# Performance work log

Measured on AMD Instinct MI355X. Metric: run time of the kernel, lower is better.

Reference implementation:

```python
import jax, jax.numpy as jnp
import numpy as np

B, T, E = 4, 2048, 1024
NH = 16
HS = E // NH  # 64


def setup_inputs() -> dict:
    key = jax.random.key(0)
    k1, k2, k3 = jax.random.split(key, 3)
    x = jax.random.normal(k1, (B, T, E), dtype=jnp.float32)
    # nn.Linear weights, stored as [in, out] so forward is x @ W
    W_attn = jax.random.normal(k2, (E, 3 * E), dtype=jnp.float32) * (1.0 / np.sqrt(E))
    W_proj = jax.random.normal(k3, (E, E), dtype=jnp.float32) * (1.0 / np.sqrt(E))
    return {"x": x, "W_attn": W_attn, "W_proj": W_proj}


def reference(x, W_attn, W_proj):
    b, t, e = x.shape
    # qkv projection; rearrange 'b t (a nh hs) -> a b nh t hs'
    qkv = x @ W_attn                                  # [b, t, 3e]
    qkv = qkv.reshape(b, t, 3, NH, HS)
    qkv = jnp.transpose(qkv, (2, 0, 3, 1, 4))          # [3, b, nh, t, hs]
    q, k, v = qkv[0], qkv[1], qkv[2]

    scale = 1.0 / np.sqrt(HS)
    # the blocked online-softmax loop in the original computes exactly
    # dense causal softmax attention
    scores = jnp.einsum('bhqd,bhkd->bhqk', q * scale, k)  # [b, nh, t, t]
    causal = jnp.tril(jnp.ones((t, t), dtype=bool))
    scores = jnp.where(causal, scores, -jnp.inf)
    p = jax.nn.softmax(scores, axis=-1)
    o = jnp.einsum('bhqk,bhkd->bhqd', p, v)            # [b, nh, t, hs]

    y = jnp.transpose(o, (0, 2, 1, 3)).reshape(b, t, e)  # 'b nh t hs -> b t (nh hs)'
    return y @ W_proj
```

## Files before the change

kernel.cpp:

```cpp
#include <hip/hip_runtime.h>
#include <hip/hip_bf16.h>
#include <cstdint>


typedef __attribute__((ext_vector_type(8))) short short8;
typedef __attribute__((ext_vector_type(4))) float f32x4;

__device__ __forceinline__ f32x4 mfma16(short8 a, short8 b, f32x4 c) {
  return __builtin_amdgcn_mfma_f32_16x16x32_bf16(a, b, c, 0, 0, 0);
}

__device__ __forceinline__ void gload16(const void* g, void* l) {
  __builtin_amdgcn_global_load_lds(
      (const __attribute__((address_space(1))) unsigned int*)g,
      (__attribute__((address_space(3))) unsigned int*)l, 16, 0, 0);
}

__device__ __forceinline__ unsigned short f2bf(float f) {
  unsigned u = __float_as_uint(f);
  u += 0x7fff + ((u >> 16) & 1);
  return (unsigned short)(u >> 16);
}

__device__ __forceinline__ float fexp2(float x) {
  float r;
  asm("v_exp_f32 %0, %1" : "=v"(r) : "v"(x));
  return r;
}

__global__ void cvt_x_kernel(const float* __restrict__ in,
                             unsigned short* __restrict__ out, int n4) {
  int i = blockIdx.x * blockDim.x + threadIdx.x;
  if (i >= n4) return;
  float4 v = ((const float4*)in)[i];
  ushort4 o;
  o.x = f2bf(v.x); o.y = f2bf(v.y); o.z = f2bf(v.z); o.w = f2bf(v.w);
  ((ushort4*)out)[i] = o;
}

__global__ void transpose_cvt_kernel(const float* __restrict__ W,
                                     unsigned short* __restrict__ Wt,
                                     int K, int N) {
  __shared__ float tile[32][33];
  int n0 = blockIdx.x * 32, k0 = blockIdx.y * 32;
  int tx = threadIdx.x, ty = threadIdx.y;
#pragma unroll
  for (int i = 0; i < 32; i += 8)
    tile[ty + i][tx] = W[(size_t)(k0 + ty + i) * N + n0 + tx];
  __syncthreads();
#pragma unroll
  for (int i = 0; i < 32; i += 8)
    Wt[(size_t)(n0 + ty + i) * K + k0 + tx] = f2bf(tile[tx][ty + i]);
}

template <int OUTF32>
__global__ __launch_bounds__(256) void gemm_bt_kernel(
    const unsigned short* __restrict__ A, const unsigned short* __restrict__ Bt,
    void* __restrict__ C, int M, int N, int K) {
  __shared__ __align__(16) unsigned short As[128 * 64];
  __shared__ __align__(16) unsigned short Bs[128 * 64];
  const int tid = threadIdx.x;
  const int lane = tid & 63;
  const int w = tid >> 6;
  const int wr = w >> 1, wc = w & 1;
  const int l15 = lane & 15, g = lane >> 4;
  const int m0 = blockIdx.x * 128, n0 = blockIdx.y * 128;

  f32x4 acc[4][4];
#pragma unroll
  for (int m = 0; m < 4; ++m)
#pragma unroll
    for (int n = 0; n < 4; ++n) acc[m][n] = (f32x4){0.f, 0.f, 0.f, 0.f};

  for (int k0 = 0; k0 < K; k0 += 64) {
    __syncthreads();
#pragma unroll
    for (int i = 0; i < 4; ++i) {
      int c = tid + 256 * i;
      int row = c >> 3;
      int piece = (c & 7) ^ (row & 7);
      gload16(A + (size_t)(m0 + row) * K + k0 + piece * 8, (char*)As + c * 16);
      gload16(Bt + (size_t)(n0 + row) * K + k0 + piece * 8, (char*)Bs + c * 16);
    }
    asm volatile("s_waitcnt vmcnt(0)" ::: "memory");
    __syncthreads();

#pragma unroll
    for (int kk = 0; kk < 2; ++kk) {
      short8 av[4], bv[4];
#pragma unroll
      for (int m = 0; m < 4; ++m) {
        int row = wr * 64 + m * 16 + l15;
        av[m] = *(const short8*)((const char*)As + row * 128 +
                                 ((kk * 64 + g * 16) ^ ((row & 7) << 4)));
      }
#pragma unroll
      for (int n = 0; n < 4; ++n) {
        int row = wc * 64 + n * 16 + l15;
        bv[n] = *(const short8*)((const char*)Bs + row * 128 +
                                 ((kk * 64 + g * 16) ^ ((row & 7) << 4)));
      }
#pragma unroll
      for (int m = 0; m < 4; ++m)
#pragma unroll
        for (int n = 0; n < 4; ++n)
          acc[m][n] = mfma16(av[m], bv[n], acc[m][n]);
    }
  }

#pragma unroll
  for (int m = 0; m < 4; ++m)
#pragma unroll
    for (int n = 0; n < 4; ++n)
#pragma unroll
      for (int r = 0; r < 4; ++r) {
        size_t row = (size_t)(m0 + wr * 64 + m * 16 + g * 4 + r);
        size_t col = (size_t)(n0 + wc * 64 + n * 16 + l15);
        if (OUTF32)
          ((float*)C)[row * N + col] = acc[m][n][r];
        else
          ((unsigned short*)C)[row * N + col] = f2bf(acc[m][n][r]);
      }
}

#define SCL 0.18033688f

__global__ __launch_bounds__(256) void attn_kernel(
    const unsigned short* __restrict__ qkv, unsigned short* __restrict__ o) {
  const int rb = blockIdx.x;
  const int lid = (rb & 7) * 128 + (rb >> 3);
  const int qt = lid & 15;
  const int bh = lid >> 4;
  const int b = bh >> 4, h = bh & 15;
  const int tid = threadIdx.x;
  const int w = tid >> 6, lane = tid & 63;
  const int l15 = lane & 15, g = lane >> 4;
  const int q0 = qt * 128;
  const int qb0 = q0 + w * 32;
  const int qb1 = qb0 + 16;

  __shared__ __align__(16) unsigned short Ks[2][64 * 64];
  __shared__ __align__(16) unsigned short Vt[2][64 * 72];
  __shared__ __align__(16) unsigned short Pl[4][32 * 72];

  const size_t row0 = (size_t)b * 2048;

  short8 qf[2][2];
#pragma unroll
  for (int u = 0; u < 2; ++u) {
    const unsigned short* qp =
        qkv + (row0 + qb0 + u * 16 + l15) * 3072 + h * 64;
#pragma unroll
    for (int c = 0; c < 2; ++c) qf[u][c] = *(const short8*)(qp + c * 32 + g * 8);
  }

  f32x4 accO[2][4];
#pragma unroll
  for (int u = 0; u < 2; ++u)
#pragma unroll
    for (int n = 0; n < 4; ++n) accO[u][n] = (f32x4){0.f, 0.f, 0.f, 0.f};
  float lsum[2] = {0.f, 0.f};

  const int kvv = (tid & 31) * 2;
  const int dv = (tid >> 5) * 8;
  const int nt = 2 * qt + 2;

  auto stageK = [&](int buf, int kt) {
#pragma unroll
    for (int i = 0; i < 2; ++i) {
      int c = tid + 256 * i;
      int row = c >> 3;
      int piece = (c & 7) ^ (row & 7);
      gload16(qkv + (row0 + kt * 64 + row) * 3072 + 1024 + h * 64 + piece * 8,
              (char*)Ks[buf] + c * 16);
    }
  };
  auto loadV = [&](int kt, short8& r0, short8& r1) {
    const unsigned short* vs =
        qkv + (row0 + kt * 64 + kvv) * 3072 + 2048 + h * 64 + dv;
    r0 = *(const short8*)vs;
    r1 = *(const short8*)(vs + 3072);
  };
  auto packV = [&](int buf, short8 r0, short8 r1) {
#pragma unroll
    for (int j = 0; j < 8; ++j) {
      unsigned pk = (unsigned)(unsigned short)r0[j] |
                    ((unsigned)(unsigned short)r1[j] << 16);
      *(unsigned*)((char*)Vt[buf] + (dv + j) * 144 + kvv * 2) = pk;
    }
  };

  short8 vr0, vr1;
  stageK(0, 0);
  loadV(0, vr0, vr1);
  asm volatile("s_waitcnt vmcnt(0)" ::: "memory");
  packV(0, vr0, vr1);

  for (int kt = 0; kt < nt; ++kt) {
    const int cur = kt & 1;
    __syncthreads();
    const bool pre = (kt + 1 < nt);
    if (pre) {
      stageK(cur ^ 1, kt + 1);
      loadV(kt + 1, vr0, vr1);
    }

    const int ktb = kt * 64;
    const bool act0 = (ktb <= qb0 + 15);
    const bool act1 = (ktb <= qb1 + 15);

    if (act1) {
      f32x4 st[2][4];
#pragma unroll
      for (int u = 0; u < 2; ++u)
#pragma unroll
        for (int tt = 0; tt < 4; ++tt) st[u][tt] = (f32x4){0.f, 0.f, 0.f, 0.f};
      const char* ksc = (const char*)Ks[cur];
#pragma unroll
      for (int tt = 0; tt < 4; ++tt) {
        int row = tt * 16 + l15;
        const char* base = ksc + row * 128;
        int sw = (row & 7) << 4;
        short8 a0 = *(const short8*)(base + ((g * 16) ^ sw));
        short8 a1 = *(const short8*)(base + ((64 + g * 16) ^ sw));
        if (act0) {
          st[0][tt] = mfma16(a0, qf[0][0], st[0][tt]);
          st[0][tt] = mfma16(a1, qf[0][1], st[0][tt]);
        }
        st[1][tt] = mfma16(a0, qf[1][0], st[1][tt]);
        st[1][tt] = mfma16(a1, qf[1][1], st[1][tt]);
      }

#pragma unroll
      for (int u = 0; u < 2; ++u) {
        const int qbu = qb0 + u * 16;
        if (ktb > qbu + 15) continue;
        const bool msk = (ktb + 63 > qbu);
        const int qq = qbu + l15;
        float part = 0.f;
#pragma unroll
        for (int tt = 0; tt < 4; ++tt) {
          float p[4];
#pragma unroll
          for (int r = 0; r < 4; ++r) {
            float s = st[u][tt][r] * SCL;
            if (msk && (ktb + tt * 16 + 4 * g + r > qq)) s = -1e30f;
            p[r] = fexp2(s);
            part += p[r];
          }
          uint2 pk;
          pk.x = (unsigned)f2bf(p[0]) | ((unsigned)f2bf(p[1]) << 16);
          pk.y = (unsigned)f2bf(p[2]) | ((unsigned)f2bf(p[3]) << 16);
          *(uint2*)((char*)Pl[w] + (u * 16 + l15) * 144 + tt * 32 + g * 8) = pk;
        }
        lsum[u] += part;
      }

#pragma unroll
      for (int c2 = 0; c2 < 2; ++c2) {
        short8 vf[4];
#pragma unroll
        for (int n = 0; n < 4; ++n)
          vf[n] = *(const short8*)((const char*)Vt[cur] +
                                   (n * 16 + l15) * 144 + c2 * 64 + g * 16);
        if (act0) {
          short8 pf0 = *(const short8*)((const char*)Pl[w] + l15 * 144 +
                                        c2 * 64 + g * 16);
#pragma unroll
          for (int n = 0; n < 4; ++n) accO[0][n] = mfma16(pf0, vf[n], accO[0][n]);
        }
        short8 pf1 = *(const short8*)((const char*)Pl[w] + (16 + l15) * 144 +
                                      c2 * 64 + g * 16);
#pragma unroll
        for (int n = 0; n < 4; ++n) accO[1][n] = mfma16(pf1, vf[n], accO[1][n]);
      }
    }

    if (pre) {
      asm volatile("s_waitcnt vmcnt(0)" ::: "memory");
      packV(cur ^ 1, vr0, vr1);
    }
  }

#pragma unroll
  for (int u = 0; u < 2; ++u) {
    float l = lsum[u];
    l += __shfl_xor(l, 16);
    l += __shfl_xor(l, 32);
    float linv[4];
#pragma unroll
    for (int r = 0; r < 4; ++r)
      linv[r] = 1.f / __shfl(l, (lane & 48) + g * 4 + r);
#pragma unroll
    for (int n = 0; n < 4; ++n)
#pragma unroll
      for (int r = 0; r < 4; ++r) {
        size_t row = row0 + qb0 + u * 16 + g * 4 + r;
        o[row * 1024 + h * 64 + n * 16 + l15] = f2bf(accO[u][n][r] * linv[r]);
      }
  }
}

extern "C" void kernel_launch(void* const* d_in, const int* in_sizes, int n_in,
                              void* d_out, int out_size, void* d_ws,
                              size_t ws_size, hipStream_t stream) {
  const float* x = (const float*)d_in[0];
  const float* W_attn = (const float*)d_in[1];
  const float* W_proj = (const float*)d_in[2];
  float* out = (float*)d_out;

  char* ws = (char*)d_ws;
  unsigned short* xb  = (unsigned short*)(ws);
  unsigned short* Wta = (unsigned short*)(ws + (16u << 20));
  unsigned short* Wtp = (unsigned short*)(ws + (22u << 20));
  unsigned short* qkv = (unsigned short*)(ws + (24u << 20));

  cvt_x_kernel<<<8192, 256, 0, stream>>>(x, xb, 8192 * 1024 / 4);
  transpose_cvt_kernel<<<dim3(96, 32), dim3(32, 8), 0, stream>>>(W_attn, Wta,
                                                                 1024, 3072);
  transpose_cvt_kernel<<<dim3(32, 32), dim3(32, 8), 0, stream>>>(W_proj, Wtp,
                                                                 1024, 1024);
  gemm_bt_kernel<0><<<dim3(64, 24), 256, 0, stream>>>(xb, Wta, qkv, 8192, 3072,
                                                      1024);
  attn_kernel<<<1024, 256, 0, stream>>>(qkv, xb);
  gemm_bt_kernel<1><<<dim3(64, 8), 256, 0, stream>>>(xb, Wtp, out, 8192, 1024,
                                                     1024);
}
```

Baseline: 283.4 us.

## Emit V transposed from QKV GEMM and restructure attention to load K/V from global

```diff
diff --git a/kernel.cpp b/kernel.cpp
--- a/kernel.cpp
+++ b/kernel.cpp
@@ -25,6 +25,12 @@
 __device__ __forceinline__ float fexp2(float x) {
   float r;
   asm("v_exp_f32 %0, %1" : "=v"(r) : "v"(x));
+  return r;
+}
+
+__device__ __forceinline__ unsigned cvtpk(float lo, float hi) {
+  unsigned r;
+  asm("v_cvt_pk_bf16_f32 %0, %1, %2" : "=v"(r) : "v"(lo), "v"(hi));
   return r;
 }
 
@@ -40,7 +46,7 @@
 
 __global__ void transpose_cvt_kernel(const float* __restrict__ W,
                                      unsigned short* __restrict__ Wt,
-                                     int K, int N) {
+                                     int K, int N, float qs, int nscale) {
   __shared__ float tile[32][33];
   int n0 = blockIdx.x * 32, k0 = blockIdx.y * 32;
   int tx = threadIdx.x, ty = threadIdx.y;
@@ -49,14 +55,19 @@
     tile[ty + i][tx] = W[(size_t)(k0 + ty + i) * N + n0 + tx];
   __syncthreads();
 #pragma unroll
-  for (int i = 0; i < 32; i += 8)
-    Wt[(size_t)(n0 + ty + i) * K + k0 + tx] = f2bf(tile[tx][ty + i]);
-}
-
-template <int OUTF32>
+  for (int i = 0; i < 32; i += 8) {
+    int n = n0 + ty + i;
+    float v = tile[tx][ty + i];
+    if (n < nscale) v *= qs;
+    Wt[(size_t)n * K + k0 + tx] = f2bf(v);
+  }
+}
+
+template <int OUTF32, int VT>
 __global__ __launch_bounds__(256) void gemm_bt_kernel(
     const unsigned short* __restrict__ A, const unsigned short* __restrict__ Bt,
-    void* __restrict__ C, int M, int N, int K) {
+    void* __restrict__ C, unsigned short* __restrict__ Cv,
+    int M, int N, int K, int ldc) {
   __shared__ __align__(16) unsigned short As[128 * 64];
   __shared__ __align__(16) unsigned short Bs[128 * 64];
   const int tid = threadIdx.x;
@@ -108,177 +119,136 @@
     }
   }
 
-#pragma unroll
-  for (int m = 0; m < 4; ++m)
-#pragma unroll
-    for (int n = 0; n < 4; ++n)
-#pragma unroll
-      for (int r = 0; r < 4; ++r) {
-        size_t row = (size_t)(m0 + wr * 64 + m * 16 + g * 4 + r);
-        size_t col = (size_t)(n0 + wc * 64 + n * 16 + l15);
-        if (OUTF32)
-          ((float*)C)[row * N + col] = acc[m][n][r];
-        else
-          ((unsigned short*)C)[row * N + col] = f2bf(acc[m][n][r]);
-      }
-}
-
-#define SCL 0.18033688f
-
-__global__ __launch_bounds__(256) void attn_kernel(
-    const unsigned short* __restrict__ qkv, unsigned short* __restrict__ o) {
+  if (!VT || n0 < 2048) {
+#pragma unroll
+    for (int m = 0; m < 4; ++m)
+#pragma unroll
+      for (int n = 0; n < 4; ++n)
+#pragma unroll
+        for (int r = 0; r < 4; ++r) {
+          size_t row = (size_t)(m0 + wr * 64 + m * 16 + g * 4 + r);
+          size_t col = (size_t)(n0 + wc * 64 + n * 16 + l15);
+          if (OUTF32)
+            ((float*)C)[row * ldc + col] = acc[m][n][r];
+          else
+            ((unsigned short*)C)[row * ldc + col] = f2bf(acc[m][n][r]);
+        }
+  } else {
+#pragma unroll
+    for (int m = 0; m < 4; ++m)
+#pragma unroll
+      for (int n = 0; n < 4; ++n)
+#pragma unroll
+        for (int r = 0; r < 4; ++r) {
+          int row = m0 + wr * 64 + m * 16 + g * 4 + r;
+          int col = n0 + wc * 64 + n * 16 + l15 - 2048;
+          int bb = row >> 11, t = row & 2047;
+          size_t dst = ((size_t)(bb * 16 + (col >> 6)) * 64 + (col & 63)) * 2048 + t;
+          Cv[dst] = f2bf(acc[m][n][r]);
+        }
+  }
+}
+
+__global__ __launch_bounds__(256, 4) void attn_kernel(
+    const unsigned short* __restrict__ qk,
+    const unsigned short* __restrict__ vt,
+    unsigned short* __restrict__ o) {
   const int rb = blockIdx.x;
-  const int lid = (rb & 7) * 128 + (rb >> 3);
-  const int qt = lid & 15;
-  const int bh = lid >> 4;
+  const int xcd = rb & 7, jj = (rb >> 3) & 31, rr = rb >> 8;
+  const int bh = xcd * 8 + (jj & 3) * 2 + (rr & 1);
+  const int pp = jj >> 2;
+  const int qt = (rr < 2) ? (15 - pp) : pp;
   const int b = bh >> 4, h = bh & 15;
   const int tid = threadIdx.x;
   const int w = tid >> 6, lane = tid & 63;
   const int l15 = lane & 15, g = lane >> 4;
-  const int q0 = qt * 128;
-  const int qb0 = q0 + w * 32;
-  const int qb1 = qb0 + 16;
-
-  __shared__ __align__(16) unsigned short Ks[2][64 * 64];
-  __shared__ __align__(16) unsigned short Vt[2][64 * 72];
+  const int qb0 = qt * 128 + w * 32;
+
   __shared__ __align__(16) unsigned short Pl[4][32 * 72];
+  char* pw = (char*)&Pl[w][0];
 
   const size_t row0 = (size_t)b * 2048;
 
   short8 qf[2][2];
 #pragma unroll
   for (int u = 0; u < 2; ++u) {
-    const unsigned short* qp =
-        qkv + (row0 + qb0 + u * 16 + l15) * 3072 + h * 64;
+    const unsigned short* qp = qk + (row0 + qb0 + u * 16 + l15) * 2048 + h * 64;
 #pragma unroll
     for (int c = 0; c < 2; ++c) qf[u][c] = *(const short8*)(qp + c * 32 + g * 8);
   }
 
-  f32x4 accO[2][4];
+  f32x4 acc[2][4];
 #pragma unroll
   for (int u = 0; u < 2; ++u)
 #pragma unroll
-    for (int n = 0; n < 4; ++n) accO[u][n] = (f32x4){0.f, 0.f, 0.f, 0.f};
+    for (int n = 0; n < 4; ++n) acc[u][n] = (f32x4){0.f, 0.f, 0.f, 0.f};
   float lsum[2] = {0.f, 0.f};
 
-  const int kvv = (tid & 31) * 2;
-  const int dv = (tid >> 5) * 8;
-  const int nt = 2 * qt + 2;
-
-  auto stageK = [&](int buf, int kt) {
-#pragma unroll
-    for (int i = 0; i < 2; ++i) {
-      int c = tid + 256 * i;
-      int row = c >> 3;
-      int piece = (c & 7) ^ (row & 7);
-      gload16(qkv + (row0 + kt * 64 + row) * 3072 + 1024 + h * 64 + piece * 8,
-              (char*)Ks[buf] + c * 16);
-    }
-  };
-  auto loadV = [&](int kt, short8& r0, short8& r1) {
-    const unsigned short* vs =
-        qkv + (row0 + kt * 64 + kvv) * 3072 + 2048 + h * 64 + dv;
-    r0 = *(const short8*)vs;
-    r1 = *(const short8*)(vs + 3072);
-  };
-  auto packV = [&](int buf, short8 r0, short8 r1) {
-#pragma unroll
-    for (int j = 0; j < 8; ++j) {
-      unsigned pk = (unsigned)(unsigned short)r0[j] |
-                    ((unsigned)(unsigned short)r1[j] << 16);
-      *(unsigned*)((char*)Vt[buf] + (dv + j) * 144 + kvv * 2) = pk;
-    }
-  };
-
-  short8 vr0, vr1;
-  stageK(0, 0);
-  loadV(0, vr0, vr1);
-  asm volatile("s_waitcnt vmcnt(0)" ::: "memory");
-  packV(0, vr0, vr1);
+  const unsigned short* kb = qk + (row0 + l15) * 2048 + 1024 + h * 64 + g * 8;
+  const unsigned short* vb = vt + ((size_t)bh * 64 + l15) * 2048 + g * 8;
+  const int nt = 2 * qt + 1 + (w >> 1);
 
   for (int kt = 0; kt < nt; ++kt) {
-    const int cur = kt & 1;
-    __syncthreads();
-    const bool pre = (kt + 1 < nt);
-    if (pre) {
-      stageK(cur ^ 1, kt + 1);
-      loadV(kt + 1, vr0, vr1);
-    }
-
     const int ktb = kt * 64;
-    const bool act0 = (ktb <= qb0 + 15);
-    const bool act1 = (ktb <= qb1 + 15);
-
-    if (act1) {
-      f32x4 st[2][4];
-#pragma unroll
-      for (int u = 0; u < 2; ++u)
-#pragma unroll
-        for (int tt = 0; tt < 4; ++tt) st[u][tt] = (f32x4){0.f, 0.f, 0.f, 0.f};
-      const char* ksc = (const char*)Ks[cur];
+    short8 kf[4][2];
+#pragma unroll
+    for (int tt = 0; tt < 4; ++tt)
+#pragma unroll
+      for (int c = 0; c < 2; ++c)
+        kf[tt][c] = *(const short8*)(kb + (size_t)(ktb + tt * 16) * 2048 + c * 32);
+
+    f32x4 st[4];
+    short8 vf[4][2];
+
+#pragma unroll
+    for (int u = 0; u < 2; ++u) {
 #pragma unroll
       for (int tt = 0; tt < 4; ++tt) {
-        int row = tt * 16 + l15;
-        const char* base = ksc + row * 128;
-        int sw = (row & 7) << 4;
-        short8 a0 = *(const short8*)(base + ((g * 16) ^ sw));
-        short8 a1 = *(const short8*)(base + ((64 + g * 16) ^ sw));
-        if (act0) {
-          st[0][tt] = mfma16(a0, qf[0][0], st[0][tt]);
-          st[0][tt] = mfma16(a1, qf[0][1], st[0][tt]);
+        st[tt] = mfma16(kf[tt][0], qf[u][0], (f32x4){0.f, 0.f, 0.f, 0.f});
+        st[tt] = mfma16(kf[tt][1], qf[u][1], st[tt]);
+      }
+      if (u == 1) {
+#pragma unroll
+        for (int n = 0; n < 4; ++n)
+#pragma unroll
+          for (int c2 = 0; c2 < 2; ++c2)
+            vf[n][c2] =
+                *(const short8*)(vb + (size_t)n * 32768 + ktb + c2 * 32);
+      }
+      const int qbu = qb0 + u * 16;
+      const bool msk = (ktb + 63 > qbu);
+      const int qq = qbu + l15;
+      float part = 0.f;
+#pragma unroll
+      for (int tt = 0; tt < 4; ++tt) {
+        float p4[4];
+#pragma unroll
+        for (int r4 = 0; r4 < 4; ++r4) {
+          float s = st[tt][r4];
+          if (msk && (ktb + tt * 16 + 4 * g + r4 > qq)) s = -1e30f;
+          float e = fexp2(s);
+          part += e;
+          p4[r4] = e;
         }
-        st[1][tt] = mfma16(a0, qf[1][0], st[1][tt]);
-        st[1][tt] = mfma16(a1, qf[1][1], st[1][tt]);
-      }
-
-#pragma unroll
-      for (int u = 0; u < 2; ++u) {
-        const int qbu = qb0 + u * 16;
-        if (ktb > qbu + 15) continue;
-        const bool msk = (ktb + 63 > qbu);
-        const int qq = qbu + l15;
-        float part = 0.f;
-#pragma unroll
-        for (int tt = 0; tt < 4; ++tt) {
-          float p[4];
-#pragma unroll
-          for (int r = 0; r < 4; ++r) {
-            float s = st[u][tt][r] * SCL;
-            if (msk && (ktb + tt * 16 + 4 * g + r > qq)) s = -1e30f;
-            p[r] = fexp2(s);
-            part += p[r];
-          }
-          uint2 pk;
-          pk.x = (unsigned)f2bf(p[0]) | ((unsigned)f2bf(p[1]) << 16);
-          pk.y = (unsigned)f2bf(p[2]) | ((unsigned)f2bf(p[3]) << 16);
-          *(uint2*)((char*)Pl[w] + (u * 16 + l15) * 144 + tt * 32 + g * 8) = pk;
-        }
-        lsum[u] += part;
-      }
-
-#pragma unroll
-      for (int c2 = 0; c2 < 2; ++c2) {
-        short8 vf[4];
-#pragma unroll
-        for (int n = 0; n < 4; ++n)
-          vf[n] = *(const short8*)((const char*)Vt[cur] +
-                                   (n * 16 + l15) * 144 + c2 * 64 + g * 16);
-        if (act0) {
-          short8 pf0 = *(const short8*)((const char*)Pl[w] + l15 * 144 +
-                                        c2 * 64 + g * 16);
-#pragma unroll
-          for (int n = 0; n < 4; ++n) accO[0][n] = mfma16(pf0, vf[n], accO[0][n]);
-        }
-        short8 pf1 = *(const short8*)((const char*)Pl[w] + (16 + l15) * 144 +
-                                      c2 * 64 + g * 16);
-#pragma unroll
-        for (int n = 0; n < 4; ++n) accO[1][n] = mfma16(pf1, vf[n], accO[1][n]);
-      }
-    }
-
-    if (pre) {
-      asm volatile("s_waitcnt vmcnt(0)" ::: "memory");
-      packV(cur ^ 1, vr0, vr1);
+        uint2 pk;
+        pk.x = cvtpk(p4[0], p4[1]);
+        pk.y = cvtpk(p4[2], p4[3]);
+        *(uint2*)(pw + (u * 16 + l15) * 144 + tt * 32 + g * 8) = pk;
+      }
+      lsum[u] += part;
+    }
+
+    asm volatile("s_waitcnt lgkmcnt(0)" ::: "memory");
+
+#pragma unroll
+    for (int c2 = 0; c2 < 2; ++c2) {
+      short8 pf0 = *(const short8*)(pw + l15 * 144 + c2 * 64 + g * 16);
+      short8 pf1 = *(const short8*)(pw + (16 + l15) * 144 + c2 * 64 + g * 16);
+#pragma unroll
+      for (int n = 0; n < 4; ++n) {
+        acc[0][n] = mfma16(pf0, vf[n][c2], acc[0][n]);
+        acc[1][n] = mfma16(pf1, vf[n][c2], acc[1][n]);
+      }
     }
   }
 
@@ -296,7 +266,7 @@
 #pragma unroll
       for (int r = 0; r < 4; ++r) {
         size_t row = row0 + qb0 + u * 16 + g * 4 + r;
-        o[row * 1024 + h * 64 + n * 16 + l15] = f2bf(accO[u][n][r] * linv[r]);
+        o[row * 1024 + h * 64 + n * 16 + l15] = f2bf(acc[u][n][r] * linv[r]);
       }
   }
 }
@@ -313,16 +283,17 @@
   unsigned short* xb  = (unsigned short*)(ws);
   unsigned short* Wta = (unsigned short*)(ws + (16u << 20));
   unsigned short* Wtp = (unsigned short*)(ws + (22u << 20));
-  unsigned short* qkv = (unsigned short*)(ws + (24u << 20));
+  unsigned short* qkb = (unsigned short*)(ws + (24u << 20));
+  unsigned short* vtb = (unsigned short*)(ws + (56u << 20));
 
   cvt_x_kernel<<<8192, 256, 0, stream>>>(x, xb, 8192 * 1024 / 4);
-  transpose_cvt_kernel<<<dim3(96, 32), dim3(32, 8), 0, stream>>>(W_attn, Wta,
-                                                                 1024, 3072);
-  transpose_cvt_kernel<<<dim3(32, 32), dim3(32, 8), 0, stream>>>(W_proj, Wtp,
-                                                                 1024, 1024);
-  gemm_bt_kernel<0><<<dim3(64, 24), 256, 0, stream>>>(xb, Wta, qkv, 8192, 3072,
-                                                      1024);
-  attn_kernel<<<1024, 256, 0, stream>>>(qkv, xb);
-  gemm_bt_kernel<1><<<dim3(64, 8), 256, 0, stream>>>(xb, Wtp, out, 8192, 1024,
-                                                     1024);
-}
+  transpose_cvt_kernel<<<dim3(96, 32), dim3(32, 8), 0, stream>>>(
+      W_attn, Wta, 1024, 3072, 0.1803368801f, 1024);
+  transpose_cvt_kernel<<<dim3(32, 32), dim3(32, 8), 0, stream>>>(
+      W_proj, Wtp, 1024, 1024, 1.0f, 0);
+  gemm_bt_kernel<0, 1><<<dim3(64, 24), 256, 0, stream>>>(
+      xb, Wta, qkb, vtb, 8192, 3072, 1024, 2048);
+  attn_kernel<<<1024, 256, 0, stream>>>(qkb, vtb, xb);
+  gemm_bt_kernel<1, 0><<<dim3(64, 8), 256, 0, stream>>>(
+      xb, Wtp, out, nullptr, 8192, 1024, 1024, 1024);
+}
```

New measurement: 346.7 us. 22.3% more time.
